# Optimization experiments

Measured on AMD Instinct MI355X. Metric: run time of the kernel, lower is better.

The kernel has to match this reference:

```python
import jax, jax.numpy as jnp
import numpy as np

B, C, H, L = 8, 1, 512, 8192


def setup_inputs() -> dict:
    key = jax.random.key(0)
    k1, k2, k3, k4 = jax.random.split(key, 4)
    u = jax.random.normal(k1, (B, H, L), dtype=jnp.float32)
    # learned SSM convolution kernel (channels, H, L); scaled so conv output is O(1)
    k = jax.random.normal(k2, (C, H, L), dtype=jnp.float32) * (1.0 / np.sqrt(L))
    D = jax.random.uniform(k3, (C, H), dtype=jnp.float32)  # skip term, as in nn.Parameter(uniform)
    W = jax.random.normal(k4, (H, C * H), dtype=jnp.float32) * (1.0 / np.sqrt(C * H))
    b = jnp.zeros((H,), dtype=jnp.float32)
    return {"u": u, "k": k, "D": D, "W": W, "b": b}


def reference(u, k, D, W, b):
    # u: (B, H, L)  k: (C, H, L)  D: (C, H)  W: (H, C*H)  b: (H,)
    Lu = u.shape[-1]
    n = 2 * Lu  # zero-padded FFT length for linear (causal) convolution
    k_f = jnp.fft.rfft(k, n=n)                       # (C, H, n//2+1) complex
    u_f = jnp.fft.rfft(u, n=n)                       # (B, H, n//2+1) complex
    y_f = jnp.einsum('bhl,chl->bchl', u_f, k_f)      # frequency-domain multiply
    y = jnp.fft.irfft(y_f, n=n)[..., :Lu]            # (B, C, H, L)
    y = y + jnp.einsum('bhl,ch->bchl', u, D)         # D skip connection
    b_, c_, h_, l_ = y.shape
    y = y.reshape(b_, c_ * h_, l_)                   # (B, C*H, L)
    y = jax.nn.gelu(y, approximate=False)            # exact-erf GELU (keras default)
    y = jnp.einsum('od,bdl->bol', W, y) + b[None, :, None]  # pointwise output linear
    return y
```

## Files before the change

### kernel.cpp

```cpp
#include <hip/hip_runtime.h>


typedef unsigned short ushort_t;
typedef __bf16 bf16x8 __attribute__((ext_vector_type(8)));
typedef float  f32x4  __attribute__((ext_vector_type(4)));

#define TWO_PI 6.283185307179586f
#define LGKM() asm volatile("s_waitcnt lgkmcnt(0)" ::: "memory")
#define CHI(p) ((((p) & 0x3C)) | (((p) + ((p) >> 4)) & 3))

__device__ __forceinline__ float2 cmulf(float2 a, float2 b) {
    return make_float2(a.x * b.x - a.y * b.y, a.x * b.y + a.y * b.x);
}
__device__ __forceinline__ float2 caddf(float2 a, float2 b) { return make_float2(a.x + b.x, a.y + b.y); }
__device__ __forceinline__ float2 csubf(float2 a, float2 b) { return make_float2(a.x - b.x, a.y - b.y); }

__device__ __forceinline__ ushort_t f2bf(float f) {
    unsigned int u = __float_as_uint(f);
    u = (u + 0x7fffu + ((u >> 16) & 1u)) >> 16;
    return (ushort_t)u;
}

__device__ __forceinline__ float gelu_exact(float x) {
    return 0.5f * x * (1.0f + erff(x * 0.70710678118654752f));
}

template<bool INV>
__device__ __forceinline__ void dft4(float2& x0, float2& x1, float2& x2, float2& x3) {
    float2 t0 = caddf(x0, x2), t1 = csubf(x0, x2);
    float2 t2 = caddf(x1, x3), t3 = csubf(x1, x3);
    x0 = caddf(t0, t2);
    x2 = csubf(t0, t2);
    if (!INV) {
        x1 = make_float2(t1.x + t3.y, t1.y - t3.x);
        x3 = make_float2(t1.x - t3.y, t1.y + t3.x);
    } else {
        x1 = make_float2(t1.x - t3.y, t1.y + t3.x);
        x3 = make_float2(t1.x + t3.y, t1.y - t3.x);
    }
}

template<bool INV>
__device__ __forceinline__ float2 cmulc(float2 a, float wr, float wi) {
    float i2 = INV ? -wi : wi;
    return make_float2(a.x * wr - a.y * i2, a.x * i2 + a.y * wr);
}

#define C1_ 0.9238795325112867f
#define S1_ 0.3826834323650898f
#define R2_ 0.7071067811865476f

template<bool INV, bool HZ>
__device__ __forceinline__ void dft16(float2* r) {
#pragma unroll
    for (int b = 0; b < 4; ++b) {
        if (HZ) {
            float2 u = r[b], v = r[4 + b];
            r[b]     = caddf(u, v);
            r[8 + b] = csubf(u, v);
            if (!INV) { r[4 + b]  = make_float2(u.x + v.y, u.y - v.x);
                        r[12 + b] = make_float2(u.x - v.y, u.y + v.x); }
            else      { r[4 + b]  = make_float2(u.x - v.y, u.y + v.x);
                        r[12 + b] = make_float2(u.x + v.y, u.y - v.x); }
        } else {
            dft4<INV>(r[b], r[4 + b], r[8 + b], r[12 + b]);
        }
    }
    r[5]  = cmulc<INV>(r[5],  C1_, -S1_);
    r[6]  = cmulc<INV>(r[6],  R2_, -R2_);
    r[7]  = cmulc<INV>(r[7],  S1_, -C1_);
    r[9]  = cmulc<INV>(r[9],  R2_, -R2_);
    r[10] = cmulc<INV>(r[10], 0.f, -1.f);
    r[11] = cmulc<INV>(r[11], -R2_, -R2_);
    r[13] = cmulc<INV>(r[13], S1_, -C1_);
    r[14] = cmulc<INV>(r[14], -R2_, -R2_);
    r[15] = cmulc<INV>(r[15], -C1_,  S1_);
    float2 o[16];
#pragma unroll
    for (int c = 0; c < 4; ++c) {
        float2 a0 = r[4*c], a1 = r[4*c+1], a2 = r[4*c+2], a3 = r[4*c+3];
        dft4<INV>(a0, a1, a2, a3);
        o[c] = a0; o[c + 4] = a1; o[c + 8] = a2; o[c + 12] = a3;
    }
#pragma unroll
    for (int i = 0; i < 16; ++i) r[i] = o[i];
}

__device__ __forceinline__ void twiddle_apply(float2* x, float theta) {
    float s, c;
    __sincosf(theta, &s, &c);
    float2 w = make_float2(c, s), wk = w;
#pragma unroll
    for (int k = 1; k < 16; ++k) { x[k] = cmulf(x[k], wk); wk = cmulf(wk, w); }
}

#define SH_SIZE 9216
#define PW_STRIDE 576

__device__ __forceinline__ void fft_fwd(float2* x, float2* SH, int t) {
    const int w  = t >> 6;
    const int d  = t & 63;
    const int kb = (t >> 2) & 15;
    const int f  = t & 3;
    float2* PW = SH + w * PW_STRIDE;
    float2 tmp[8];
    const bool tlo = (t < 512);

    dft16<false, true>(x);
    twiddle_apply(x, -TWO_PI * (float)t * (1.0f / 16384.0f));

    if (tlo) {
#pragma unroll
        for (int r = 0; r < 16; ++r) SH[r * 512 + t] = x[r];
    }
    __syncthreads();
#pragma unroll
    for (int c = 0; c < 8; ++c) {
        float2 v = SH[w * 512 + c * 64 + d];
        if (tlo) x[c] = v; else tmp[c] = v;
    }
    __syncthreads();
    if (!tlo) {
#pragma unroll
        for (int r = 0; r < 16; ++r) SH[r * 512 + (t - 512)] = x[r];
    }
    __syncthreads();
#pragma unroll
    for (int c = 8; c < 16; ++c) x[c] = SH[w * 512 + (c - 8) * 64 + d];
    if (!tlo) {
#pragma unroll
        for (int c = 0; c < 8; ++c) x[c] = tmp[c];
    }

    dft16<false, false>(x);
    twiddle_apply(x, -TWO_PI * (float)d * (1.0f / 1024.0f));
    __syncthreads();

    {
        const bool dlo = (d < 32);
        const int dc = d & 31;
        if (dlo) {
#pragma unroll
            for (int r = 0; r < 16; ++r) PW[r * 36 + dc] = x[r];
        }
        LGKM();
#pragma unroll
        for (int e = 0; e < 8; ++e) {
            float2 v = PW[kb * 36 + e * 4 + f];
            if (dlo) x[e] = v; else tmp[e] = v;
        }
        LGKM();
        if (!dlo) {
#pragma unroll
            for (int r = 0; r < 16; ++r) PW[r * 36 + dc] = x[r];
        }
        LGKM();
#pragma unroll
        for (int e = 8; e < 16; ++e) x[e] = PW[kb * 36 + (e - 8) * 4 + f];
        if (!dlo) {
#pragma unroll
            for (int e = 0; e < 8; ++e) x[e] = tmp[e];
        }
    }

    dft16<false, false>(x);
    twiddle_apply(x, -TWO_PI * (float)f * (1.0f / 64.0f));

    {
        const int row = (kb & 7) * 68;
        const bool klo = (kb < 8);
        if (klo) {
#pragma unroll
            for (int r = 0; r < 16; ++r) PW[row + CHI(r * 4 + f)] = x[r];
        }
        LGKM();
        if (klo) {
#pragma unroll
            for (int q = 0; q < 4; ++q)
#pragma unroll
                for (int ff = 0; ff < 4; ++ff)
                    x[q * 4 + ff] = PW[row + CHI(f * 16 + q * 4 + ff)];
        }
        LGKM();
        if (!klo) {
#pragma unroll
            for (int r = 0; r < 16; ++r) PW[row + CHI(r * 4 + f)] = x[r];
        }
        LGKM();
        if (!klo) {
#pragma unroll
            for (int q = 0; q < 4; ++q)
#pragma unroll
                for (int ff = 0; ff < 4; ++ff)
                    x[q * 4 + ff] = PW[row + CHI(f * 16 + q * 4 + ff)];
        }
    }

#pragma unroll
    for (int q = 0; q < 4; ++q) dft4<false>(x[4*q], x[4*q+1], x[4*q+2], x[4*q+3]);
}

__device__ __forceinline__ void fft_inv(float2* x, float2* SH, int t) {
    const int w  = t >> 6;
    const int d  = t & 63;
    const int kb = (t >> 2) & 15;
    const int f  = t & 3;
    float2* PW = SH + w * PW_STRIDE;
    float2 tmp[8];

#pragma unroll
    for (int q = 0; q < 4; ++q) dft4<true>(x[4*q], x[4*q+1], x[4*q+2], x[4*q+3]);

    {
        const int row = (kb & 7) * 68;
        const bool klo = (kb < 8);
        LGKM();
        if (klo) {
#pragma unroll
            for (int q = 0; q < 4; ++q)
#pragma unroll
                for (int ff = 0; ff < 4; ++ff)
                    PW[row + CHI(f * 16 + q * 4 + ff)] = x[q * 4 + ff];
        }
        LGKM();
        if (klo) {
#pragma unroll
            for (int r = 0; r < 16; ++r) x[r] = PW[row + CHI(r * 4 + f)];
        }
        LGKM();
        if (!klo) {
#pragma unroll
            for (int q = 0; q < 4; ++q)
#pragma unroll
                for (int ff = 0; ff < 4; ++ff)
                    PW[row + CHI(f * 16 + q * 4 + ff)] = x[q * 4 + ff];
        }
        LGKM();
        if (!klo) {
#pragma unroll
            for (int r = 0; r < 16; ++r) x[r] = PW[row + CHI(r * 4 + f)];
        }
    }

    twiddle_apply(x, TWO_PI * (float)f * (1.0f / 64.0f));
    dft16<true, false>(x);

    {
        const int row = (kb & 7) * 68;
        const bool klo = (kb < 8);
        LGKM();
        if (klo) {
#pragma unroll
            for (int e = 0; e < 16; ++e) PW[row + CHI(e * 4 + f)] = x[e];
        }
        LGKM();
#pragma unroll
        for (int r = 0; r < 8; ++r) {
            float2 v = PW[r * 68 + CHI(d)];
            if (klo) x[r] = v; else tmp[r] = v;
        }
        LGKM();
        if (!klo) {
#pragma unroll
            for (int e = 0; e < 16; ++e) PW[row + CHI(e * 4 + f)] = x[e];
        }
        LGKM();
#pragma unroll
        for (int r = 8; r < 16; ++r) x[r] = PW[(r - 8) * 68 + CHI(d)];
        if (!klo) {
#pragma unroll
            for (int r = 0; r < 8; ++r) x[r] = tmp[r];
        }
    }

    twiddle_apply(x, TWO_PI * (float)d * (1.0f / 1024.0f));
    dft16<true, false>(x);

    __syncthreads();
    if (w < 8) {
#pragma unroll
        for (int c = 0; c < 16; ++c) SH[w * 1024 + c * 64 + d] = x[c];
    }
    __syncthreads();
#pragma unroll
    for (int r = 0; r < 8; ++r) {
        float2 v = SH[r * 1024 + t];
        if (w < 8) x[r] = v; else tmp[r] = v;
    }
    __syncthreads();
    if (w >= 8) {
#pragma unroll
        for (int c = 0; c < 16; ++c) SH[(w - 8) * 1024 + c * 64 + d] = x[c];
    }
    __syncthreads();
#pragma unroll
    for (int r = 8; r < 16; ++r) x[r] = SH[(r - 8) * 1024 + t];
    if (w >= 8) {
#pragma unroll
        for (int r = 0; r < 8; ++r) x[r] = tmp[r];
    }

    twiddle_apply(x, TWO_PI * (float)t * (1.0f / 16384.0f));
    dft16<true, false>(x);
}

__global__ void wconv(const float* __restrict__ W, ushort_t* __restrict__ Wb, int n)
{
    int i = blockIdx.x * 256 + threadIdx.x;
    if (i < n) Wb[i] = f2bf(W[i]);
}

__global__ __launch_bounds__(1024, 1) void kf_build(const float* __restrict__ k,
                                                    const float* __restrict__ D,
                                                    float2* __restrict__ Kf)
{
    __shared__ float2 SH[SH_SIZE];
    int h = blockIdx.x, t = threadIdx.x;
    const float* kr = k + (size_t)h * 8192;
    float2 x[16];
#pragma unroll
    for (int a = 0; a < 8; ++a) x[a] = make_float2(kr[a * 1024 + t], 0.f);
#pragma unroll
    for (int a = 8; a < 16; ++a) x[a] = make_float2(0.f, 0.f);
    fft_fwd(x, SH, t);
    float dh = D[h];
    float2* o = Kf + (size_t)h * 16384;
#pragma unroll
    for (int r = 0; r < 16; ++r) {
        float2 z = x[r];
        z.x += dh;
        o[r * 1024 + t] = z;
    }
}

__global__ __launch_bounds__(1024, 1) void conv_gelu(const float* __restrict__ u,
                                                     const float2* __restrict__ Kf,
                                                     ushort_t* __restrict__ g)
{
    __shared__ float2 SH[SH_SIZE];
    int h    = blockIdx.x;
    int pair = blockIdx.y;
    int b0   = pair * 2;
    int t    = threadIdx.x;
    const float* u0 = u + ((size_t)(b0 * 512 + h)) * 8192;
    const float* u1 = u0 + (size_t)512 * 8192;
    float2 x[16];
#pragma unroll
    for (int a = 0; a < 8; ++a) x[a] = make_float2(u0[a * 1024 + t], u1[a * 1024 + t]);
#pragma unroll
    for (int a = 8; a < 16; ++a) x[a] = make_float2(0.f, 0.f);
    fft_fwd(x, SH, t);
    const float2* kf = Kf + (size_t)blockIdx.x * 16384;
#pragma unroll
    for (int r = 0; r < 16; ++r) x[r] = cmulf(x[r], kf[r * 1024 + t]);
    fft_inv(x, SH, t);
    const float sc = 1.0f / 16384.0f;
    ushort_t* g0 = g + ((size_t)(b0 * 512 + blockIdx.x)) * 8192;
    ushort_t* g1 = g0 + (size_t)512 * 8192;
#pragma unroll
    for (int a = 0; a < 8; ++a) {
        int n = a * 1024 + t;
        g0[n] = f2bf(gelu_exact(x[a].x * sc));
        g1[n] = f2bf(gelu_exact(x[a].y * sc));
    }
}

__global__ __launch_bounds__(256) void transpose_g(const ushort_t* __restrict__ g,
                                                   ushort_t* __restrict__ gT)
{
    __shared__ ushort_t TL[64][68];
    int lt = blockIdx.x;
    int ht = blockIdx.y;
    int b  = blockIdx.z;
    int t  = threadIdx.x;
    int l0 = lt * 64, h0 = ht * 64;
#pragma unroll
    for (int i = 0; i < 4; ++i) {
        int c   = t + (i << 8);
        int row = c >> 4;
        int col = (c & 15) * 4;
        const ushort_t* src = g + ((size_t)(b * 512 + h0 + row)) * 8192 + l0 + col;
        ushort4 v = *(const ushort4*)src;
        TL[col + 0][row] = v.x;
        TL[col + 1][row] = v.y;
        TL[col + 2][row] = v.z;
        TL[col + 3][row] = v.w;
    }
    __syncthreads();
#pragma unroll
    for (int i = 0; i < 4; ++i) {
        int c    = t + (i << 8);
        int lrow = c >> 4;
        int hcol = (c & 15) * 4;
        ushort4 v = *(const ushort4*)&TL[lrow][hcol];
        *(ushort4*)(gT + ((size_t)b * 8192 + l0 + lrow) * 512 + h0 + hcol) = v;
    }
}

__global__ __launch_bounds__(256, 2) void gemm_out(const ushort_t* __restrict__ Wb,
                                                   const ushort_t* __restrict__ gT,
                                                   const float* __restrict__ bias,
                                                   float* __restrict__ out)
{
    __shared__ __align__(16) ushort_t As[128 * 32];
    __shared__ __align__(16) ushort_t Bs[128 * 32];
    int lt = blockIdx.x;
    int ot = blockIdx.y;
    int b  = blockIdx.z;
    int l0 = lt * 128, o0 = ot * 128;
    int t    = threadIdx.x;
    int wave = t >> 6, lid = t & 63;
    int wm = wave >> 1, wn = wave & 1;
    int q  = lid >> 4, mi = lid & 15;

    f32x4 acc[4][4];
#pragma unroll
    for (int i = 0; i < 4; ++i)
#pragma unroll
        for (int j = 0; j < 4; ++j)
            acc[i][j] = (f32x4){0.f, 0.f, 0.f, 0.f};

    const size_t gTb = (size_t)b * 8192 * 512;
    for (int it = 0; it < 16; ++it) {
        int k0 = it * 32;
        __syncthreads();
#pragma unroll
        for (int i = 0; i < 2; ++i) {
            int ch  = t + (i << 8);
            int row = ch >> 2;
            int kc  = (ch & 3) << 3;
            uint4 va = *(const uint4*)(Wb + (size_t)(o0 + row) * 512 + k0 + kc);
            *(uint4*)&As[row * 32 + kc] = va;
            uint4 vb = *(const uint4*)(gT + gTb + (size_t)(l0 + row) * 512 + k0 + kc);
            *(uint4*)&Bs[row * 32 + kc] = vb;
        }
        __syncthreads();
        bf16x8 af[4], bfr[4];
#pragma unroll
        for (int ff = 0; ff < 4; ++ff) {
            af[ff]  = *(const bf16x8*)&As[(wm * 64 + ff * 16 + mi) * 32 + q * 8];
            bfr[ff] = *(const bf16x8*)&Bs[(wn * 64 + ff * 16 + mi) * 32 + q * 8];
        }
#pragma unroll
        for (int i = 0; i < 4; ++i)
#pragma unroll
            for (int j = 0; j < 4; ++j)
                acc[i][j] = __builtin_amdgcn_mfma_f32_16x16x32_bf16(af[i], bfr[j], acc[i][j], 0, 0, 0);
    }

#pragma unroll
    for (int i = 0; i < 4; ++i) {
        int o_base = o0 + wm * 64 + i * 16 + q * 4;
#pragma unroll
        for (int j = 0; j < 4; ++j) {
            int l = l0 + wn * 64 + j * 16 + mi;
#pragma unroll
            for (int r = 0; r < 4; ++r) {
                int o = o_base + r;
                out[((size_t)b * 512 + o) * 8192 + l] = acc[i][j][r] + bias[o];
            }
        }
    }
}

extern "C" void kernel_launch(void* const* d_in, const int* in_sizes, int n_in,
                              void* d_out, int out_size, void* d_ws, size_t ws_size,
                              hipStream_t stream)
{
    (void)in_sizes; (void)n_in; (void)out_size; (void)ws_size;
    const float* u    = (const float*)d_in[0];
    const float* k    = (const float*)d_in[1];
    const float* D    = (const float*)d_in[2];
    const float* W    = (const float*)d_in[3];
    const float* bias = (const float*)d_in[4];
    float* out = (float*)d_out;

    char* ws = (char*)d_ws;
    float2*   Kf = (float2*)ws;
    ushort_t* gT = (ushort_t*)(ws + 67108864);
    ushort_t* Wb = (ushort_t*)(ws + 134217728);
    ushort_t* g  = (ushort_t*)d_out;

    wconv<<<1024, 256, 0, stream>>>(W, Wb, 512 * 512);
    kf_build<<<512, 1024, 0, stream>>>(k, D, Kf);
    conv_gelu<<<dim3(512, 4), 1024, 0, stream>>>(u, Kf, g);
    transpose_g<<<dim3(128, 8, 8), 256, 0, stream>>>(g, gT);
    gemm_out<<<dim3(64, 4, 8), 256, 0, stream>>>(Wb, gT, bias, out);
}
```

Measured before the change: 478.6 us.

## Fold transpose into GEMM B-tile load and swizzle block order

Removes the separate transpose kernel. The GEMM now reads the bf16 activation in its natural (H, L) layout and transposes it through a padded shared-memory tile, gathering the MFMA B fragments with scalar ushort LDS reads. The grid is flattened with a block-index remap, likely aimed at XCD/L2 locality. This saves a full read and write of the 64 MB intermediate, at the cost of eight 2-byte LDS reads per fragment instead of one vector read.

```diff
diff --git a/kernel.cpp b/kernel.cpp
--- a/kernel.cpp
+++ b/kernel.cpp
@@ -4,6 +4,7 @@
 typedef unsigned short ushort_t;
 typedef __bf16 bf16x8 __attribute__((ext_vector_type(8)));
 typedef float  f32x4  __attribute__((ext_vector_type(4)));
+typedef unsigned short ushort8 __attribute__((ext_vector_type(8)));
 
 #define TWO_PI 6.283185307179586f
 #define LGKM() asm volatile("s_waitcnt lgkmcnt(0)" ::: "memory")
@@ -365,48 +366,21 @@
     }
 }
 
-__global__ __launch_bounds__(256) void transpose_g(const ushort_t* __restrict__ g,
-                                                   ushort_t* __restrict__ gT)
-{
-    __shared__ ushort_t TL[64][68];
-    int lt = blockIdx.x;
-    int ht = blockIdx.y;
-    int b  = blockIdx.z;
-    int t  = threadIdx.x;
-    int l0 = lt * 64, h0 = ht * 64;
-#pragma unroll
-    for (int i = 0; i < 4; ++i) {
-        int c   = t + (i << 8);
-        int row = c >> 4;
-        int col = (c & 15) * 4;
-        const ushort_t* src = g + ((size_t)(b * 512 + h0 + row)) * 8192 + l0 + col;
-        ushort4 v = *(const ushort4*)src;
-        TL[col + 0][row] = v.x;
-        TL[col + 1][row] = v.y;
-        TL[col + 2][row] = v.z;
-        TL[col + 3][row] = v.w;
-    }
-    __syncthreads();
-#pragma unroll
-    for (int i = 0; i < 4; ++i) {
-        int c    = t + (i << 8);
-        int lrow = c >> 4;
-        int hcol = (c & 15) * 4;
-        ushort4 v = *(const ushort4*)&TL[lrow][hcol];
-        *(ushort4*)(gT + ((size_t)b * 8192 + l0 + lrow) * 512 + h0 + hcol) = v;
-    }
-}
+#define BIDX(k, l) ((k) * 144 + (((k) >> 3) & 3) * 16 + (l))
 
 __global__ __launch_bounds__(256, 2) void gemm_out(const ushort_t* __restrict__ Wb,
-                                                   const ushort_t* __restrict__ gT,
+                                                   const ushort_t* __restrict__ g,
                                                    const float* __restrict__ bias,
                                                    float* __restrict__ out)
 {
     __shared__ __align__(16) ushort_t As[128 * 32];
-    __shared__ __align__(16) ushort_t Bs[128 * 32];
-    int lt = blockIdx.x;
-    int ot = blockIdx.y;
-    int b  = blockIdx.z;
+    __shared__ __align__(16) ushort_t Bs2[4640];
+
+    int bid     = blockIdx.x;
+    int logical = (bid & 7) * 256 + (bid >> 3);
+    int ot = logical & 3;
+    int lt = (logical >> 2) & 63;
+    int b  = logical >> 8;
     int l0 = lt * 128, o0 = ot * 128;
     int t    = threadIdx.x;
     int wave = t >> 6, lid = t & 63;
@@ -420,26 +394,32 @@
         for (int j = 0; j < 4; ++j)
             acc[i][j] = (f32x4){0.f, 0.f, 0.f, 0.f};
 
-    const size_t gTb = (size_t)b * 8192 * 512;
+    const ushort_t* gb = g + (size_t)b * 512 * 8192;
     for (int it = 0; it < 16; ++it) {
         int k0 = it * 32;
         __syncthreads();
 #pragma unroll
         for (int i = 0; i < 2; ++i) {
-            int ch  = t + (i << 8);
-            int row = ch >> 2;
-            int kc  = (ch & 3) << 3;
-            uint4 va = *(const uint4*)(Wb + (size_t)(o0 + row) * 512 + k0 + kc);
-            *(uint4*)&As[row * 32 + kc] = va;
-            uint4 vb = *(const uint4*)(gT + gTb + (size_t)(l0 + row) * 512 + k0 + kc);
-            *(uint4*)&Bs[row * 32 + kc] = vb;
+            int ch = t + (i << 8);
+            int arow = ch >> 2;
+            int akc  = (ch & 3) << 3;
+            uint4 va = *(const uint4*)(Wb + (size_t)(o0 + arow) * 512 + k0 + akc);
+            *(uint4*)&As[arow * 32 + akc] = va;
+            int hr = ch >> 4;
+            int lc = ch & 15;
+            uint4 vb = *(const uint4*)(gb + (size_t)(k0 + hr) * 8192 + l0 + (lc << 3));
+            *(uint4*)&Bs2[BIDX(hr, lc << 3)] = vb;
         }
         __syncthreads();
         bf16x8 af[4], bfr[4];
 #pragma unroll
         for (int ff = 0; ff < 4; ++ff) {
-            af[ff]  = *(const bf16x8*)&As[(wm * 64 + ff * 16 + mi) * 32 + q * 8];
-            bfr[ff] = *(const bf16x8*)&Bs[(wn * 64 + ff * 16 + mi) * 32 + q * 8];
+            af[ff] = *(const bf16x8*)&As[(wm * 64 + ff * 16 + mi) * 32 + q * 8];
+            ushort8 bu;
+#pragma unroll
+            for (int j = 0; j < 8; ++j)
+                bu[j] = Bs2[BIDX(q * 8 + j, wn * 64 + ff * 16 + mi)];
+            bfr[ff] = __builtin_bit_cast(bf16x8, bu);
         }
 #pragma unroll
         for (int i = 0; i < 4; ++i)
@@ -477,13 +457,11 @@
 
     char* ws = (char*)d_ws;
     float2*   Kf = (float2*)ws;
-    ushort_t* gT = (ushort_t*)(ws + 67108864);
+    ushort_t* g  = (ushort_t*)(ws + 67108864);
     ushort_t* Wb = (ushort_t*)(ws + 134217728);
-    ushort_t* g  = (ushort_t*)d_out;
 
     wconv<<<1024, 256, 0, stream>>>(W, Wb, 512 * 512);
     kf_build<<<512, 1024, 0, stream>>>(k, D, Kf);
     conv_gelu<<<dim3(512, 4), 1024, 0, stream>>>(u, Kf, g);
-    transpose_g<<<dim3(128, 8, 8), 256, 0, stream>>>(g, gT);
-    gemm_out<<<dim3(64, 4, 8), 256, 0, stream>>>(Wb, gT, bias, out);
-}
+    gemm_out<<<2048, 256, 0, stream>>>(Wb, g, bias, out);
+}
```

After: 485.2 us. Within noise of the previous version (+1.4%).
